# Performance work log

Measured on AMD Instinct MI355X. Metric: run time of the kernel, lower is better.

The kernel has to match this reference:

```python
import jax, jax.numpy as jnp
import numpy as np

B, N, T, F = 256, 64, 50, 2
E, H, R = 64, 128, 30


def setup_inputs() -> dict:
    key = jax.random.key(0)
    ks = jax.random.split(key, 16)
    rn = lambda k, shp, s=0.1: jax.random.normal(k, shp, jnp.float32) * s
    return {
        "src": jax.random.normal(ks[0], (B, N, T, F), jnp.float32),
        "trg": jax.random.normal(ks[1], (B, R, F), jnp.float32),
        # spatial encoder: residual Linear (no bias) + GCNConv weight/bias
        "W_res": rn(ks[2], (F, E)),
        "W_gcn": rn(ks[3], (F, E)),
        "b_gcn": jnp.zeros((E,), jnp.float32),
        # encoder LSTMCell (PyTorch gate order i,f,g,o); b = b_ih + b_hh fused
        "W_ih_e": rn(ks[4], (E, 4 * H)),
        "W_hh_e": rn(ks[5], (H, 4 * H)),
        "b_e": jnp.zeros((4 * H,), jnp.float32),
        # decoder: linear1 (2->E), LSTMCell (E->H), linear2 (H->2)
        "W1": rn(ks[6], (F, E)),
        "b1": jnp.zeros((E,), jnp.float32),
        "W_ih_d": rn(ks[7], (E, 4 * H)),
        "W_hh_d": rn(ks[8], (H, 4 * H)),
        "b_d": jnp.zeros((4 * H,), jnp.float32),
        "W2": rn(ks[9], (H, F)),
        "b2": jnp.zeros((F,), jnp.float32),
    }


def _lstm_step(h, c, xt, W_ih, W_hh, b):
    g = xt @ W_ih + h @ W_hh + b
    i, f, gg, o = jnp.split(g, 4, axis=-1)
    c = jax.nn.sigmoid(f) * c + jax.nn.sigmoid(i) * jnp.tanh(gg)
    h = jax.nn.sigmoid(o) * jnp.tanh(c)
    return h, c


def _forward(src, trg, W_res, W_gcn, b_gcn, W_ih_e, W_hh_e, b_e,
             W1, b1, W_ih_d, W_hh_d, b_d, W2, b2):
    # ---- EncoderSpatial: distance-weighted GCNConv over per-(sample,t) full graph ----
    x = jnp.swapaxes(src, 1, 2)                       # [B,T,N,F]
    diff = x[:, :, :, None, :] - x[:, :, None, :, :]  # [B,T,N,N,F]
    dist = jnp.linalg.norm(diff, axis=-1)             # [B,T,N,N]
    dist = jnp.where(dist == 0.0, 1e-6, dist)
    w = jnp.minimum(1.0 / dist, 1.0)                  # clipped inverse distance
    eye = jnp.eye(N, dtype=x.dtype)
    w = w * (1.0 - eye) + eye                         # remove self loops, GCN adds them with weight 1
    dinv = jnp.sum(w, axis=-1) ** -0.5                # [B,T,N]
    A = w * dinv[..., :, None] * dinv[..., None, :]   # sym-normalized adjacency
    gcn = jnp.einsum('btij,btjf->btif', A, x @ W_gcn) + b_gcn
    enc = jax.nn.relu(gcn + x @ W_res)                # [B,T,N,E]
    emb = enc[:, :, 0, :]                             # target-agent embeddings [B,T,E]
    inputs0 = x[:, :, 0, :]                           # target-agent positions  [B,T,F]

    # ---- LSTM encoder over T steps ----
    def enc_step(carry, xt):
        h, c = _lstm_step(carry[0], carry[1], xt, W_ih_e, W_hh_e, b_e)
        return (h, c), None
    h0 = jnp.zeros((B, H), src.dtype)
    (h, c), _ = jax.lax.scan(enc_step, (h0, h0), jnp.swapaxes(emb, 0, 1))

    def dec_step(carry, _):
        xin, h, c = carry
        ed = jax.nn.relu(xin @ W1 + b1)
        h, c = _lstm_step(h, c, ed, W_ih_d, W_hh_d, b_d)
        out = h @ W2 + b2
        return (out, h, c), out
    (_, _, _), outs = jax.lax.scan(dec_step, (inputs0[:, -1, :], h, c), None, length=R)
    return jnp.swapaxes(outs, 0, 1)                   # reg: [B,R,F]


def reference(src, trg, W_res, W_gcn, b_gcn, W_ih_e, W_hh_e, b_e,
              W1, b1, W_ih_d, W_hh_d, b_d, W2, b2):
    return _forward(src, trg, W_res, W_gcn, b_gcn, W_ih_e, W_hh_e, b_e,
                    W1, b1, W_ih_d, W_hh_d, b_d, W2, b2)
```

## Files before the change

### kernel.cpp

```cpp
#include <hip/hip_runtime.h>

#define Bn 256
#define Nn 64
#define Tn 50
#define Fn 2
#define En 64
#define Hn 128
#define Rn 30
#define G4 512
#define EMS 6416

typedef _Float16 h2    __attribute__((ext_vector_type(2)));
typedef _Float16 f16x8 __attribute__((ext_vector_type(8)));
typedef float    f32x4 __attribute__((ext_vector_type(4)));

__device__ __forceinline__ float sigf(float x) {
    return __builtin_amdgcn_rcpf(1.0f + __expf(-x));
}
__device__ __forceinline__ float tanh_fast(float x) {
    return 1.0f - 2.0f * __builtin_amdgcn_rcpf(__expf(2.0f * x) + 1.0f);
}
__device__ __forceinline__ h2 pack2(float a, float b) {
    h2 r; r[0] = (_Float16)a; r[1] = (_Float16)b; return r;
}

__device__ __forceinline__ void blockbar() {
    __builtin_amdgcn_sched_barrier(0);
    asm volatile("s_waitcnt lgkmcnt(0)" ::: "memory");
    __builtin_amdgcn_s_barrier();
    __builtin_amdgcn_sched_barrier(0);
}

__global__ __launch_bounds__(512) void k_emb(const float* __restrict__ src,
                                             const float* __restrict__ W_res,
                                             const float* __restrict__ W_gcn,
                                             const float* __restrict__ b_gcn,
                                             _Float16* __restrict__ emb)
{
    const int lane = threadIdx.x & 63;
    const int wv   = threadIdx.x >> 6;
    const int task = blockIdx.x * 8 + wv;
    const int b = task / Tn;
    const int t = task - b * Tn;

    __shared__ float2 xs[8][Nn];

    const float2 xv = *reinterpret_cast<const float2*>(
        src + (((size_t)b * Nn + lane) * Tn + t) * Fn);
    const float x0 = xv.x, x1 = xv.y;
    xs[wv][lane] = xv;

    float rowsum = 0.0f, w0 = 0.0f;
    #pragma unroll
    for (int k = 0; k < Nn; k++) {
        const float2 o = xs[wv][k];
        const float dx = x0 - o.x, dy = x1 - o.y;
        const float w = fminf(__builtin_amdgcn_rsqf(dx * dx + dy * dy), 1.0f);
        rowsum += w;
        if (k == 0) w0 = w;
    }
    const float dinv  = __builtin_amdgcn_rsqf(rowsum);
    const float dinv0 = __shfl(dinv, 0);
    const float a = w0 * dinv0 * dinv;

    float p0 = a * x0, p1 = a * x1;
    #pragma unroll
    for (int off = 32; off; off >>= 1) {
        p0 += __shfl_xor(p0, off);
        p1 += __shfl_xor(p1, off);
    }
    const float xa = __shfl(x0, 0);
    const float xb = __shfl(x1, 0);

    const float v = p0 * W_gcn[lane] + p1 * W_gcn[En + lane] + b_gcn[lane]
                  + xa * W_res[lane] + xb * W_res[En + lane];
    emb[(size_t)task * En + lane] = (_Float16)fmaxf(v, 0.0f);
}

__global__ __launch_bounds__(512) void k_seq(
    const _Float16* __restrict__ emb,
    const float* __restrict__ src,
    const float* __restrict__ W_hh_e, const float* __restrict__ W_ih_e,
    const float* __restrict__ b_e,
    const float* __restrict__ W1,     const float* __restrict__ b1,
    const float* __restrict__ W_ih_d, const float* __restrict__ W_hh_d,
    const float* __restrict__ b_d,
    const float* __restrict__ W2,     const float* __restrict__ b2,
    float* __restrict__ out)
{
    const int tid  = threadIdx.x;
    const int lane = tid & 63;
    const int wv   = tid >> 6;
    const int l15  = lane & 15;
    const int lg   = lane >> 4;
    const int cc   = wv * 16 + l15;
    const int bq0  = blockIdx.x * 4;
    const int mb   = l15 & 3;

    __shared__ __align__(16) _Float16 hbuf[2][576];
    __shared__ __align__(16) _Float16 wi_frag[8 * 8 * 64 * 8];
    __shared__ __align__(16) _Float16 emb_lds[4 * 3208];
    __shared__ __align__(16) float    redw[2][8][4][2];

    char* const embbase = reinterpret_cast<char*>(&emb_lds[0]);

    f16x8 bfr[4][4];
    #pragma unroll
    for (int g = 0; g < 4; g++)
        #pragma unroll
        for (int kt = 0; kt < 4; kt++) {
            f16x8 v;
            #pragma unroll
            for (int j = 0; j < 8; j++)
                v[j] = (_Float16)W_hh_e[(size_t)(kt * 32 + lg * 8 + j) * G4 + g * 128 + cc];
            bfr[g][kt] = v;
        }

    #pragma unroll
    for (int g = 0; g < 4; g++)
        #pragma unroll
        for (int kt2 = 0; kt2 < 2; kt2++) {
            f16x8 v;
            #pragma unroll
            for (int j = 0; j < 8; j++)
                v[j] = (_Float16)W_ih_e[(size_t)(kt2 * 32 + lg * 8 + j) * G4 + g * 128 + cc];
            *reinterpret_cast<f16x8*>(&wi_frag[((wv * 8 + g * 2 + kt2) * 64 + lane) * 8]) = v;
        }

    {
        const _Float16* eg = emb + (size_t)bq0 * Tn * En;
        for (int i = tid; i < 1600; i += 512) {
            const int m = i / 400;
            const int r = i - m * 400;
            const uint4 v = *reinterpret_cast<const uint4*>(eg + i * 8);
            *reinterpret_cast<uint4*>(embbase + m * EMS + r * 16) = v;
        }
    }

    if (tid < 288) reinterpret_cast<float*>(&hbuf[0][0])[tid] = 0.0f;

    const float be0 = b_e[cc], be1 = b_e[128 + cc], be2 = b_e[256 + cc], be3 = b_e[384 + cc];

    float cst = 0.0f;
    char* const hb0 = reinterpret_cast<char*>(&hbuf[0][0]);
    char* const hb1 = reinterpret_cast<char*>(&hbuf[1][0]);
    __syncthreads();

    for (int t = 0; t < Tn; t++) {
        const int cur = t & 1;
        char* const hr = cur ? hb1 : hb0;
        char* const hw = cur ? hb0 : hb1;

        f16x8 af[4];
        #pragma unroll
        for (int kt = 0; kt < 4; kt++)
            af[kt] = *reinterpret_cast<const f16x8*>(
                hr + (l15 & 3) * 288 + kt * 64 + lg * 16);
        f16x8 ae[2];
        #pragma unroll
        for (int kt2 = 0; kt2 < 2; kt2++)
            ae[kt2] = *reinterpret_cast<const f16x8*>(
                embbase + mb * EMS + t * 128 + kt2 * 64 + lg * 16);

        f32x4 acc[4] = {};
        #pragma unroll
        for (int kt = 0; kt < 4; kt++)
            #pragma unroll
            for (int g = 0; g < 4; g++)
                acc[g] = __builtin_amdgcn_mfma_f32_16x16x32_f16(af[kt], bfr[g][kt], acc[g], 0, 0, 0);
        #pragma unroll
        for (int g = 0; g < 4; g++)
            #pragma unroll
            for (int kt2 = 0; kt2 < 2; kt2++) {
                const f16x8 bfe = *reinterpret_cast<const f16x8*>(
                    &wi_frag[((wv * 8 + g * 2 + kt2) * 64 + lane) * 8]);
                acc[g] = __builtin_amdgcn_mfma_f32_16x16x32_f16(ae[kt2], bfe, acc[g], 0, 0, 0);
            }

        float ga[4];
        #pragma unroll
        for (int g = 0; g < 4; g++) {
            const float s01 = (lg & 1) ? acc[g][1] : acc[g][0];
            const float s23 = (lg & 1) ? acc[g][3] : acc[g][2];
            ga[g] = (lg & 2) ? s23 : s01;
        }

        const float gi = ga[0] + be0;
        const float gf = ga[1] + be1;
        const float gg = ga[2] + be2;
        const float go = ga[3] + be3;
        cst = sigf(gf) * cst + sigf(gi) * tanh_fast(gg);
        const float hv = sigf(go) * tanh_fast(cst);

        *reinterpret_cast<_Float16*>(hw + lg * 288 + cc * 2) = (_Float16)hv;
        blockbar();
    }

    #pragma unroll
    for (int g = 0; g < 4; g++)
        #pragma unroll
        for (int kt = 0; kt < 4; kt++) {
            f16x8 v;
            #pragma unroll
            for (int j = 0; j < 8; j++)
                v[j] = (_Float16)W_hh_d[(size_t)(kt * 32 + lg * 8 + j) * G4 + g * 128 + cc];
            bfr[g][kt] = v;
        }
    #pragma unroll
    for (int g = 0; g < 4; g++)
        #pragma unroll
        for (int kt2 = 0; kt2 < 2; kt2++) {
            f16x8 v;
            #pragma unroll
            for (int j = 0; j < 8; j++)
                v[j] = (_Float16)W_ih_d[(size_t)(kt2 * 32 + lg * 8 + j) * G4 + g * 128 + cc];
            *reinterpret_cast<f16x8*>(&wi_frag[((wv * 8 + g * 2 + kt2) * 64 + lane) * 8]) = v;
        }

    const float bd0 = b_d[cc], bd1 = b_d[128 + cc], bd2 = b_d[256 + cc], bd3 = b_d[384 + cc];
    const float w2a = W2[cc * 2], w2b = W2[cc * 2 + 1];
    const float b20 = b2[0], b21 = b2[1];

    h2 w1ah[8], w1bh[8], b1h[8];
    #pragma unroll
    for (int q = 0; q < 8; q++) {
        const int e0 = (q >> 2) * 32 + lg * 8 + (q & 3) * 2;
        w1ah[q] = pack2(W1[e0],      W1[e0 + 1]);
        w1bh[q] = pack2(W1[En + e0], W1[En + e0 + 1]);
        b1h[q]  = pack2(b1[e0],      b1[e0 + 1]);
    }

    float o0 = src[((size_t)(bq0 + mb) * Nn * Tn + (Tn - 1)) * Fn + 0];
    float o1 = src[((size_t)(bq0 + mb) * Nn * Tn + (Tn - 1)) * Fn + 1];
    __syncthreads();

    for (int r = 0; r < Rn; r++) {
        const int cur = r & 1;
        char* const hr = cur ? hb1 : hb0;
        char* const hw = cur ? hb0 : hb1;

        const h2 o0h = pack2(o0, o0);
        const h2 o1h = pack2(o1, o1);
        f16x8 ae[2];
        #pragma unroll
        for (int kt2 = 0; kt2 < 2; kt2++)
            #pragma unroll
            for (int p = 0; p < 4; p++) {
                h2 v = w1ah[kt2 * 4 + p] * o0h + w1bh[kt2 * 4 + p] * o1h + b1h[kt2 * 4 + p];
                v[0] = v[0] > (_Float16)0 ? v[0] : (_Float16)0;
                v[1] = v[1] > (_Float16)0 ? v[1] : (_Float16)0;
                ae[kt2][2 * p]     = v[0];
                ae[kt2][2 * p + 1] = v[1];
            }

        f16x8 af[4];
        #pragma unroll
        for (int kt = 0; kt < 4; kt++)
            af[kt] = *reinterpret_cast<const f16x8*>(
                hr + (l15 & 3) * 288 + kt * 64 + lg * 16);

        f32x4 acc[4] = {};
        #pragma unroll
        for (int kt = 0; kt < 4; kt++)
            #pragma unroll
            for (int g = 0; g < 4; g++)
                acc[g] = __builtin_amdgcn_mfma_f32_16x16x32_f16(af[kt], bfr[g][kt], acc[g], 0, 0, 0);
        #pragma unroll
        for (int g = 0; g < 4; g++)
            #pragma unroll
            for (int kt2 = 0; kt2 < 2; kt2++) {
                const f16x8 bfe = *reinterpret_cast<const f16x8*>(
                    &wi_frag[((wv * 8 + g * 2 + kt2) * 64 + lane) * 8]);
                acc[g] = __builtin_amdgcn_mfma_f32_16x16x32_f16(ae[kt2], bfe, acc[g], 0, 0, 0);
            }

        float ga[4];
        #pragma unroll
        for (int g = 0; g < 4; g++) {
            const float s01 = (lg & 1) ? acc[g][1] : acc[g][0];
            const float s23 = (lg & 1) ? acc[g][3] : acc[g][2];
            ga[g] = (lg & 2) ? s23 : s01;
        }

        const float gi = ga[0] + bd0;
        const float gf = ga[1] + bd1;
        const float gg = ga[2] + bd2;
        const float go = ga[3] + bd3;
        cst = sigf(gf) * cst + sigf(gi) * tanh_fast(gg);
        const float hv = sigf(go) * tanh_fast(cst);
        *reinterpret_cast<_Float16*>(hw + lg * 288 + cc * 2) = (_Float16)hv;

        float p0 = hv * w2a, p1 = hv * w2b;
        #pragma unroll
        for (int off = 1; off < 16; off <<= 1) {
            p0 += __shfl_xor(p0, off);
            p1 += __shfl_xor(p1, off);
        }
        if (l15 == 0) {
            redw[cur][wv][lg][0] = p0;
            redw[cur][wv][lg][1] = p1;
        }
        blockbar();

        o0 = b20; o1 = b21;
        #pragma unroll
        for (int w8 = 0; w8 < 8; w8++) {
            const float2 rr = *reinterpret_cast<const float2*>(&redw[cur][w8][mb][0]);
            o0 += rr.x; o1 += rr.y;
        }
        if (wv == 4 && l15 < 2) {
            float oo = l15 ? b21 : b20;
            #pragma unroll
            for (int w8 = 0; w8 < 8; w8++) oo += redw[cur][w8][lg][l15];
            out[(((size_t)(bq0 + lg)) * Rn + r) * Fn + l15] = oo;
        }
    }
}

extern "C" void kernel_launch(void* const* d_in, const int* in_sizes, int n_in,
                              void* d_out, int out_size, void* d_ws, size_t ws_size,
                              hipStream_t stream)
{
    const float* src    = (const float*)d_in[0];
    const float* W_res  = (const float*)d_in[2];
    const float* W_gcn  = (const float*)d_in[3];
    const float* b_gcn  = (const float*)d_in[4];
    const float* W_ih_e = (const float*)d_in[5];
    const float* W_hh_e = (const float*)d_in[6];
    const float* b_e    = (const float*)d_in[7];
    const float* W1     = (const float*)d_in[8];
    const float* b1     = (const float*)d_in[9];
    const float* W_ih_d = (const float*)d_in[10];
    const float* W_hh_d = (const float*)d_in[11];
    const float* b_d    = (const float*)d_in[12];
    const float* W2     = (const float*)d_in[13];
    const float* b2     = (const float*)d_in[14];

    float* out = (float*)d_out;
    _Float16* emb = (_Float16*)d_ws;

    k_emb<<<(Bn * Tn) / 8, 512, 0, stream>>>(src, W_res, W_gcn, b_gcn, emb);
    k_seq<<<Bn / 4, 512, 0, stream>>>(emb, src,
                                      W_hh_e, W_ih_e, b_e,
                                      W1, b1,
                                      W_ih_d, W_hh_d, b_d,
                                      W2, b2, out);
}
```

Baseline: 90.44 us.

## Fuse embedding and LSTM kernels with per-group atomic counters for overlap

```diff
diff --git a/kernel.cpp b/kernel.cpp
--- a/kernel.cpp
+++ b/kernel.cpp
@@ -31,101 +31,117 @@
     __builtin_amdgcn_sched_barrier(0);
 }
 
-__global__ __launch_bounds__(512) void k_emb(const float* __restrict__ src,
-                                             const float* __restrict__ W_res,
-                                             const float* __restrict__ W_gcn,
-                                             const float* __restrict__ b_gcn,
-                                             _Float16* __restrict__ emb)
-{
-    const int lane = threadIdx.x & 63;
-    const int wv   = threadIdx.x >> 6;
-    const int task = blockIdx.x * 8 + wv;
-    const int b = task / Tn;
-    const int t = task - b * Tn;
-
-    __shared__ float2 xs[8][Nn];
-
-    const float2 xv = *reinterpret_cast<const float2*>(
-        src + (((size_t)b * Nn + lane) * Tn + t) * Fn);
-    const float x0 = xv.x, x1 = xv.y;
-    xs[wv][lane] = xv;
-
-    float rowsum = 0.0f, w0 = 0.0f;
-    #pragma unroll
-    for (int k = 0; k < Nn; k++) {
-        const float2 o = xs[wv][k];
-        const float dx = x0 - o.x, dy = x1 - o.y;
-        const float w = fminf(__builtin_amdgcn_rsqf(dx * dx + dy * dy), 1.0f);
-        rowsum += w;
-        if (k == 0) w0 = w;
-    }
-    const float dinv  = __builtin_amdgcn_rsqf(rowsum);
-    const float dinv0 = __shfl(dinv, 0);
-    const float a = w0 * dinv0 * dinv;
-
-    float p0 = a * x0, p1 = a * x1;
-    #pragma unroll
-    for (int off = 32; off; off >>= 1) {
-        p0 += __shfl_xor(p0, off);
-        p1 += __shfl_xor(p1, off);
-    }
-    const float xa = __shfl(x0, 0);
-    const float xb = __shfl(x1, 0);
-
-    const float v = p0 * W_gcn[lane] + p1 * W_gcn[En + lane] + b_gcn[lane]
-                  + xa * W_res[lane] + xb * W_res[En + lane];
-    emb[(size_t)task * En + lane] = (_Float16)fmaxf(v, 0.0f);
-}
-
-__global__ __launch_bounds__(512) void k_seq(
-    const _Float16* __restrict__ emb,
+__global__ __launch_bounds__(512) void k_fused(
     const float* __restrict__ src,
+    const float* __restrict__ W_res,  const float* __restrict__ W_gcn,
+    const float* __restrict__ b_gcn,
     const float* __restrict__ W_hh_e, const float* __restrict__ W_ih_e,
     const float* __restrict__ b_e,
     const float* __restrict__ W1,     const float* __restrict__ b1,
     const float* __restrict__ W_ih_d, const float* __restrict__ W_hh_d,
     const float* __restrict__ b_d,
     const float* __restrict__ W2,     const float* __restrict__ b2,
+    unsigned int* __restrict__ ctr,
+    _Float16* __restrict__ emb,
     float* __restrict__ out)
 {
     const int tid  = threadIdx.x;
     const int lane = tid & 63;
     const int wv   = tid >> 6;
-    const int l15  = lane & 15;
-    const int lg   = lane >> 4;
-    const int cc   = wv * 16 + l15;
-    const int bq0  = blockIdx.x * 4;
-    const int mb   = l15 & 3;
 
     __shared__ __align__(16) _Float16 hbuf[2][576];
     __shared__ __align__(16) _Float16 wi_frag[8 * 8 * 64 * 8];
     __shared__ __align__(16) _Float16 emb_lds[4 * 3208];
     __shared__ __align__(16) float    redw[2][8][4][2];
 
+    if (blockIdx.x >= 64) {
+        const int e    = blockIdx.x - 64;
+        const int task = e * 8 + wv;
+        const int b    = task / Tn;
+        const int t    = task - b * Tn;
+
+        float2* xs = reinterpret_cast<float2*>(&emb_lds[0]) + wv * Nn;
+
+        const float2 xv = *reinterpret_cast<const float2*>(
+            src + (((size_t)b * Nn + lane) * Tn + t) * Fn);
+        const float x0 = xv.x, x1 = xv.y;
+        xs[lane] = xv;
+
+        float rowsum = 0.0f, w0 = 0.0f;
+        #pragma unroll
+        for (int k = 0; k < Nn; k++) {
+            const float2 o = xs[k];
+            const float dx = x0 - o.x, dy = x1 - o.y;
+            const float w = fminf(__builtin_amdgcn_rsqf(dx * dx + dy * dy), 1.0f);
+            rowsum += w;
+            if (k == 0) w0 = w;
+        }
+        const float dinv  = __builtin_amdgcn_rsqf(rowsum);
+        const float dinv0 = __shfl(dinv, 0);
+        const float a = w0 * dinv0 * dinv;
+
+        float p0 = a * x0, p1 = a * x1;
+        #pragma unroll
+        for (int off = 32; off; off >>= 1) {
+            p0 += __shfl_xor(p0, off);
+            p1 += __shfl_xor(p1, off);
+        }
+        const float xa = __shfl(x0, 0);
+        const float xb = __shfl(x1, 0);
+
+        const float v = p0 * W_gcn[lane] + p1 * W_gcn[En + lane] + b_gcn[lane]
+                      + xa * W_res[lane] + xb * W_res[En + lane];
+        emb[(size_t)task * En + lane] = (_Float16)fmaxf(v, 0.0f);
+
+        __syncthreads();
+        if (tid == 0) {
+            __threadfence();
+            atomicAdd(&ctr[e / 25], 1u);
+        }
+        return;
+    }
+
+    const int l15  = lane & 15;
+    const int lg   = lane >> 4;
+    const int cc   = wv * 16 + l15;
+    const int g    = blockIdx.x;
+    const int bq0  = g * 4;
+    const int mb   = l15 & 3;
+
     char* const embbase = reinterpret_cast<char*>(&emb_lds[0]);
 
     f16x8 bfr[4][4];
     #pragma unroll
-    for (int g = 0; g < 4; g++)
+    for (int gg = 0; gg < 4; gg++)
         #pragma unroll
         for (int kt = 0; kt < 4; kt++) {
             f16x8 v;
             #pragma unroll
             for (int j = 0; j < 8; j++)
-                v[j] = (_Float16)W_hh_e[(size_t)(kt * 32 + lg * 8 + j) * G4 + g * 128 + cc];
-            bfr[g][kt] = v;
-        }
-
-    #pragma unroll
-    for (int g = 0; g < 4; g++)
+                v[j] = (_Float16)W_hh_e[(size_t)(kt * 32 + lg * 8 + j) * G4 + gg * 128 + cc];
+            bfr[gg][kt] = v;
+        }
+
+    #pragma unroll
+    for (int gg = 0; gg < 4; gg++)
         #pragma unroll
         for (int kt2 = 0; kt2 < 2; kt2++) {
             f16x8 v;
             #pragma unroll
             for (int j = 0; j < 8; j++)
-                v[j] = (_Float16)W_ih_e[(size_t)(kt2 * 32 + lg * 8 + j) * G4 + g * 128 + cc];
-            *reinterpret_cast<f16x8*>(&wi_frag[((wv * 8 + g * 2 + kt2) * 64 + lane) * 8]) = v;
-        }
+                v[j] = (_Float16)W_ih_e[(size_t)(kt2 * 32 + lg * 8 + j) * G4 + gg * 128 + cc];
+            *reinterpret_cast<f16x8*>(&wi_frag[((wv * 8 + gg * 2 + kt2) * 64 + lane) * 8]) = v;
+        }
+
+    if (tid < 288) reinterpret_cast<float*>(&hbuf[0][0])[tid] = 0.0f;
+
+    const float be0 = b_e[cc], be1 = b_e[128 + cc], be2 = b_e[256 + cc], be3 = b_e[384 + cc];
+
+    if (tid == 0) {
+        while (atomicAdd(&ctr[g], 0u) < 25u) __builtin_amdgcn_s_sleep(2);
+        __threadfence();
+    }
+    __syncthreads();
 
     {
         const _Float16* eg = emb + (size_t)bq0 * Tn * En;
@@ -137,13 +153,12 @@
         }
     }
 
-    if (tid < 288) reinterpret_cast<float*>(&hbuf[0][0])[tid] = 0.0f;
-
-    const float be0 = b_e[cc], be1 = b_e[128 + cc], be2 = b_e[256 + cc], be3 = b_e[384 + cc];
-
     float cst = 0.0f;
     char* const hb0 = reinterpret_cast<char*>(&hbuf[0][0]);
     char* const hb1 = reinterpret_cast<char*>(&hbuf[1][0]);
+    const int afo = (l15 & 3) * 288 + lg * 16;
+    const int aeo = mb * EMS + lg * 16;
+    const int hwo = lg * 288 + cc * 2;
     __syncthreads();
 
     for (int t = 0; t < Tn; t++) {
@@ -154,67 +169,65 @@
         f16x8 af[4];
         #pragma unroll
         for (int kt = 0; kt < 4; kt++)
-            af[kt] = *reinterpret_cast<const f16x8*>(
-                hr + (l15 & 3) * 288 + kt * 64 + lg * 16);
+            af[kt] = *reinterpret_cast<const f16x8*>(hr + afo + kt * 64);
         f16x8 ae[2];
         #pragma unroll
         for (int kt2 = 0; kt2 < 2; kt2++)
-            ae[kt2] = *reinterpret_cast<const f16x8*>(
-                embbase + mb * EMS + t * 128 + kt2 * 64 + lg * 16);
+            ae[kt2] = *reinterpret_cast<const f16x8*>(embbase + aeo + t * 128 + kt2 * 64);
 
         f32x4 acc[4] = {};
         #pragma unroll
         for (int kt = 0; kt < 4; kt++)
             #pragma unroll
-            for (int g = 0; g < 4; g++)
-                acc[g] = __builtin_amdgcn_mfma_f32_16x16x32_f16(af[kt], bfr[g][kt], acc[g], 0, 0, 0);
-        #pragma unroll
-        for (int g = 0; g < 4; g++)
+            for (int gg = 0; gg < 4; gg++)
+                acc[gg] = __builtin_amdgcn_mfma_f32_16x16x32_f16(af[kt], bfr[gg][kt], acc[gg], 0, 0, 0);
+        #pragma unroll
+        for (int gg = 0; gg < 4; gg++)
             #pragma unroll
             for (int kt2 = 0; kt2 < 2; kt2++) {
                 const f16x8 bfe = *reinterpret_cast<const f16x8*>(
-                    &wi_frag[((wv * 8 + g * 2 + kt2) * 64 + lane) * 8]);
-                acc[g] = __builtin_amdgcn_mfma_f32_16x16x32_f16(ae[kt2], bfe, acc[g], 0, 0, 0);
+                    &wi_frag[((wv * 8 + gg * 2 + kt2) * 64 + lane) * 8]);
+                acc[gg] = __builtin_amdgcn_mfma_f32_16x16x32_f16(ae[kt2], bfe, acc[gg], 0, 0, 0);
             }
 
         float ga[4];
         #pragma unroll
-        for (int g = 0; g < 4; g++) {
-            const float s01 = (lg & 1) ? acc[g][1] : acc[g][0];
-            const float s23 = (lg & 1) ? acc[g][3] : acc[g][2];
-            ga[g] = (lg & 2) ? s23 : s01;
+        for (int gg = 0; gg < 4; gg++) {
+            const float s01 = (lg & 1) ? acc[gg][1] : acc[gg][0];
+            const float s23 = (lg & 1) ? acc[gg][3] : acc[gg][2];
+            ga[gg] = (lg & 2) ? s23 : s01;
         }
 
         const float gi = ga[0] + be0;
         const float gf = ga[1] + be1;
-        const float gg = ga[2] + be2;
+        const float gG = ga[2] + be2;
         const float go = ga[3] + be3;
-        cst = sigf(gf) * cst + sigf(gi) * tanh_fast(gg);
+        cst = sigf(gf) * cst + sigf(gi) * tanh_fast(gG);
         const float hv = sigf(go) * tanh_fast(cst);
 
-        *reinterpret_cast<_Float16*>(hw + lg * 288 + cc * 2) = (_Float16)hv;
+        *reinterpret_cast<_Float16*>(hw + hwo) = (_Float16)hv;
         blockbar();
     }
 
     #pragma unroll
-    for (int g = 0; g < 4; g++)
+    for (int gg = 0; gg < 4; gg++)
         #pragma unroll
         for (int kt = 0; kt < 4; kt++) {
             f16x8 v;
             #pragma unroll
             for (int j = 0; j < 8; j++)
-                v[j] = (_Float16)W_hh_d[(size_t)(kt * 32 + lg * 8 + j) * G4 + g * 128 + cc];
-            bfr[g][kt] = v;
-        }
-    #pragma unroll
-    for (int g = 0; g < 4; g++)
+                v[j] = (_Float16)W_hh_d[(size_t)(kt * 32 + lg * 8 + j) * G4 + gg * 128 + cc];
+            bfr[gg][kt] = v;
+        }
+    #pragma unroll
+    for (int gg = 0; gg < 4; gg++)
         #pragma unroll
         for (int kt2 = 0; kt2 < 2; kt2++) {
             f16x8 v;
             #pragma unroll
             for (int j = 0; j < 8; j++)
-                v[j] = (_Float16)W_ih_d[(size_t)(kt2 * 32 + lg * 8 + j) * G4 + g * 128 + cc];
-            *reinterpret_cast<f16x8*>(&wi_frag[((wv * 8 + g * 2 + kt2) * 64 + lane) * 8]) = v;
+                v[j] = (_Float16)W_ih_d[(size_t)(kt2 * 32 + lg * 8 + j) * G4 + gg * 128 + cc];
+            *reinterpret_cast<f16x8*>(&wi_frag[((wv * 8 + gg * 2 + kt2) * 64 + lane) * 8]) = v;
         }
 
     const float bd0 = b_d[cc], bd1 = b_d[128 + cc], bd2 = b_d[256 + cc], bd3 = b_d[384 + cc];
@@ -256,39 +269,38 @@
         f16x8 af[4];
         #pragma unroll
         for (int kt = 0; kt < 4; kt++)
-            af[kt] = *reinterpret_cast<const f16x8*>(
-                hr + (l15 & 3) * 288 + kt * 64 + lg * 16);
+            af[kt] = *reinterpret_cast<const f16x8*>(hr + afo + kt * 64);
 
         f32x4 acc[4] = {};
         #pragma unroll
         for (int kt = 0; kt < 4; kt++)
             #pragma unroll
-            for (int g = 0; g < 4; g++)
-                acc[g] = __builtin_amdgcn_mfma_f32_16x16x32_f16(af[kt], bfr[g][kt], acc[g], 0, 0, 0);
-        #pragma unroll
-        for (int g = 0; g < 4; g++)
+            for (int gg = 0; gg < 4; gg++)
+                acc[gg] = __builtin_amdgcn_mfma_f32_16x16x32_f16(af[kt], bfr[gg][kt], acc[gg], 0, 0, 0);
+        #pragma unroll
+        for (int gg = 0; gg < 4; gg++)
             #pragma unroll
             for (int kt2 = 0; kt2 < 2; kt2++) {
                 const f16x8 bfe = *reinterpret_cast<const f16x8*>(
-                    &wi_frag[((wv * 8 + g * 2 + kt2) * 64 + lane) * 8]);
-                acc[g] = __builtin_amdgcn_mfma_f32_16x16x32_f16(ae[kt2], bfe, acc[g], 0, 0, 0);
+                    &wi_frag[((wv * 8 + gg * 2 + kt2) * 64 + lane) * 8]);
+                acc[gg] = __builtin_amdgcn_mfma_f32_16x16x32_f16(ae[kt2], bfe, acc[gg], 0, 0, 0);
             }
 
         float ga[4];
         #pragma unroll
-        for (int g = 0; g < 4; g++) {
-            const float s01 = (lg & 1) ? acc[g][1] : acc[g][0];
-            const float s23 = (lg & 1) ? acc[g][3] : acc[g][2];
-            ga[g] = (lg & 2) ? s23 : s01;
+        for (int gg = 0; gg < 4; gg++) {
+            const float s01 = (lg & 1) ? acc[gg][1] : acc[gg][0];
+            const float s23 = (lg & 1) ? acc[gg][3] : acc[gg][2];
+            ga[gg] = (lg & 2) ? s23 : s01;
         }
 
         const float gi = ga[0] + bd0;
         const float gf = ga[1] + bd1;
-        const float gg = ga[2] + bd2;
+        const float gG = ga[2] + bd2;
         const float go = ga[3] + bd3;
-        cst = sigf(gf) * cst + sigf(gi) * tanh_fast(gg);
+        cst = sigf(gf) * cst + sigf(gi) * tanh_fast(gG);
         const float hv = sigf(go) * tanh_fast(cst);
-        *reinterpret_cast<_Float16*>(hw + lg * 288 + cc * 2) = (_Float16)hv;
+        *reinterpret_cast<_Float16*>(hw + hwo) = (_Float16)hv;
 
         float p0 = hv * w2a, p1 = hv * w2b;
         #pragma unroll
@@ -337,12 +349,15 @@
     const float* b2     = (const float*)d_in[14];
 
     float* out = (float*)d_out;
-    _Float16* emb = (_Float16*)d_ws;
-
-    k_emb<<<(Bn * Tn) / 8, 512, 0, stream>>>(src, W_res, W_gcn, b_gcn, emb);
-    k_seq<<<Bn / 4, 512, 0, stream>>>(emb, src,
-                                      W_hh_e, W_ih_e, b_e,
-                                      W1, b1,
-                                      W_ih_d, W_hh_d, b_d,
-                                      W2, b2, out);
-}
+    unsigned int* ctr = (unsigned int*)d_ws;
+    _Float16* emb = (_Float16*)((char*)d_ws + 256);
+
+    hipMemsetAsync(d_ws, 0, 256, stream);
+    k_fused<<<64 + (Bn * Tn) / 8, 512, 0, stream>>>(
+        src, W_res, W_gcn, b_gcn,
+        W_hh_e, W_ih_e, b_e,
+        W1, b1,
+        W_ih_d, W_hh_d, b_d,
+        W2, b2,
+        ctr, emb, out);
+}
```

Result: slower. 153.2 us (+69.4%).

## Restructure embedding kernel to one block per batch with coalesced shared-memory transpose

Applied to the files above, without the earlier changes.

```diff
diff --git a/kernel.cpp b/kernel.cpp
--- a/kernel.cpp
+++ b/kernel.cpp
@@ -37,44 +37,55 @@
                                              const float* __restrict__ b_gcn,
                                              _Float16* __restrict__ emb)
 {
-    const int lane = threadIdx.x & 63;
-    const int wv   = threadIdx.x >> 6;
-    const int task = blockIdx.x * 8 + wv;
-    const int b = task / Tn;
-    const int t = task - b * Tn;
-
-    __shared__ float2 xs[8][Nn];
-
-    const float2 xv = *reinterpret_cast<const float2*>(
-        src + (((size_t)b * Nn + lane) * Tn + t) * Fn);
-    const float x0 = xv.x, x1 = xv.y;
-    xs[wv][lane] = xv;
-
-    float rowsum = 0.0f, w0 = 0.0f;
-    #pragma unroll
-    for (int k = 0; k < Nn; k++) {
-        const float2 o = xs[wv][k];
-        const float dx = x0 - o.x, dy = x1 - o.y;
-        const float w = fminf(__builtin_amdgcn_rsqf(dx * dx + dy * dy), 1.0f);
-        rowsum += w;
-        if (k == 0) w0 = w;
-    }
-    const float dinv  = __builtin_amdgcn_rsqf(rowsum);
-    const float dinv0 = __shfl(dinv, 0);
-    const float a = w0 * dinv0 * dinv;
-
-    float p0 = a * x0, p1 = a * x1;
-    #pragma unroll
-    for (int off = 32; off; off >>= 1) {
-        p0 += __shfl_xor(p0, off);
-        p1 += __shfl_xor(p1, off);
-    }
-    const float xa = __shfl(x0, 0);
-    const float xb = __shfl(x1, 0);
-
-    const float v = p0 * W_gcn[lane] + p1 * W_gcn[En + lane] + b_gcn[lane]
-                  + xa * W_res[lane] + xb * W_res[En + lane];
-    emb[(size_t)task * En + lane] = (_Float16)fmaxf(v, 0.0f);
+    const int tid  = threadIdx.x;
+    const int lane = tid & 63;
+    const int wv   = tid >> 6;
+    const int b    = blockIdx.x;
+
+    __shared__ float2 xt[Tn * 65];
+
+    const float2* s2 = reinterpret_cast<const float2*>(src + (size_t)b * Nn * Tn * Fn);
+    for (int i = tid; i < Nn * Tn; i += 512) {
+        const int n = i / Tn;
+        const int t = i - n * Tn;
+        xt[t * 65 + n] = s2[i];
+    }
+
+    const float wg0 = W_gcn[lane], wg1 = W_gcn[En + lane];
+    const float wr0 = W_res[lane], wr1 = W_res[En + lane];
+    const float bg  = b_gcn[lane];
+    __syncthreads();
+
+    for (int t = wv; t < Tn; t += 8) {
+        const float2* row = &xt[t * 65];
+        const float2 xv = row[lane];
+        const float x0 = xv.x, x1 = xv.y;
+
+        float rowsum = 0.0f, w0 = 0.0f;
+        #pragma unroll
+        for (int k = 0; k < Nn; k++) {
+            const float2 o = row[k];
+            const float dx = x0 - o.x, dy = x1 - o.y;
+            const float w = fminf(__builtin_amdgcn_rsqf(dx * dx + dy * dy), 1.0f);
+            rowsum += w;
+            if (k == 0) w0 = w;
+        }
+        const float dinv  = __builtin_amdgcn_rsqf(rowsum);
+        const float dinv0 = __shfl(dinv, 0);
+        const float a = w0 * dinv0 * dinv;
+
+        float p0 = a * x0, p1 = a * x1;
+        #pragma unroll
+        for (int off = 32; off; off >>= 1) {
+            p0 += __shfl_xor(p0, off);
+            p1 += __shfl_xor(p1, off);
+        }
+        const float xa = __shfl(x0, 0);
+        const float xb = __shfl(x1, 0);
+
+        const float v = p0 * wg0 + p1 * wg1 + bg + xa * wr0 + xb * wr1;
+        emb[((size_t)b * Tn + t) * En + lane] = (_Float16)fmaxf(v, 0.0f);
+    }
 }
 
 __global__ __launch_bounds__(512) void k_seq(
@@ -144,6 +155,9 @@
     float cst = 0.0f;
     char* const hb0 = reinterpret_cast<char*>(&hbuf[0][0]);
     char* const hb1 = reinterpret_cast<char*>(&hbuf[1][0]);
+    const int afo = (l15 & 3) * 288 + lg * 16;
+    const int aeo = mb * EMS + lg * 16;
+    const int hwo = lg * 288 + cc * 2;
     __syncthreads();
 
     for (int t = 0; t < Tn; t++) {
@@ -154,13 +168,11 @@
         f16x8 af[4];
         #pragma unroll
         for (int kt = 0; kt < 4; kt++)
-            af[kt] = *reinterpret_cast<const f16x8*>(
-                hr + (l15 & 3) * 288 + kt * 64 + lg * 16);
+            af[kt] = *reinterpret_cast<const f16x8*>(hr + afo + kt * 64);
         f16x8 ae[2];
         #pragma unroll
         for (int kt2 = 0; kt2 < 2; kt2++)
-            ae[kt2] = *reinterpret_cast<const f16x8*>(
-                embbase + mb * EMS + t * 128 + kt2 * 64 + lg * 16);
+            ae[kt2] = *reinterpret_cast<const f16x8*>(embbase + aeo + t * 128 + kt2 * 64);
 
         f32x4 acc[4] = {};
         #pragma unroll
@@ -192,7 +204,7 @@
         cst = sigf(gf) * cst + sigf(gi) * tanh_fast(gg);
         const float hv = sigf(go) * tanh_fast(cst);
 
-        *reinterpret_cast<_Float16*>(hw + lg * 288 + cc * 2) = (_Float16)hv;
+        *reinterpret_cast<_Float16*>(hw + hwo) = (_Float16)hv;
         blockbar();
     }
 
@@ -256,8 +268,7 @@
         f16x8 af[4];
         #pragma unroll
         for (int kt = 0; kt < 4; kt++)
-            af[kt] = *reinterpret_cast<const f16x8*>(
-                hr + (l15 & 3) * 288 + kt * 64 + lg * 16);
+            af[kt] = *reinterpret_cast<const f16x8*>(hr + afo + kt * 64);
 
         f32x4 acc[4] = {};
         #pragma unroll
@@ -288,7 +299,7 @@
         const float go = ga[3] + bd3;
         cst = sigf(gf) * cst + sigf(gi) * tanh_fast(gg);
         const float hv = sigf(go) * tanh_fast(cst);
-        *reinterpret_cast<_Float16*>(hw + lg * 288 + cc * 2) = (_Float16)hv;
+        *reinterpret_cast<_Float16*>(hw + hwo) = (_Float16)hv;
 
         float p0 = hv * w2a, p1 = hv * w2b;
         #pragma unroll
@@ -339,7 +350,7 @@
     float* out = (float*)d_out;
     _Float16* emb = (_Float16*)d_ws;
 
-    k_emb<<<(Bn * Tn) / 8, 512, 0, stream>>>(src, W_res, W_gcn, b_gcn, emb);
+    k_emb<<<Bn, 512, 0, stream>>>(src, W_res, W_gcn, b_gcn, emb);
     k_seq<<<Bn / 4, 512, 0, stream>>>(emb, src,
                                       W_hh_e, W_ih_e, b_e,
                                       W1, b1,
```

New measurement: 94.24 us. +4.2%, slower.
